# Kernel optimization log

Hardware: AMD Instinct MI355X
Metric: run time of the kernel (lower is better)

Reference implementation:

```python
import jax, jax.numpy as jnp
import numpy as np

N, K, FIN, FOUT = 50000, 32, 128, 128

def setup_inputs() -> dict:
    key = jax.random.key(0)
    k1, k2, k3 = jax.random.split(key, 3)
    x = jax.random.normal(k1, (N, FIN), dtype=jnp.float32)
    nbrs = jax.random.randint(k2, (N, K), 0, N)
    # nn.Linear weight init scale ~ 1/sqrt(fan_in)
    W = jax.random.normal(k3, (FIN, FOUT), dtype=jnp.float32) / np.sqrt(FIN).astype(np.float32)
    return {"x": x, "nbrs": nbrs, "W": W}

def reference(x, nbrs, W):
    # h = self.w(x)  (bias=False)
    h = x @ W                              # [N, FOUT]
    g = jnp.take(h, nbrs, axis=0)          # [N, K, FOUT] gather of neighbor features
    s = jnp.sort(g, axis=1)                # sort each neighbor list per feature
    k = nbrs.shape[1]
    # torch.median returns the lower median: sorted[(k-1)//2]
    return s[:, (k - 1) // 2, :]           # [N, FOUT]
```

## Files before the change

kernel.cpp:

```cpp
#include <hip/hip_runtime.h>

#define FIN 128
#define FOUT 128
#define KNB 32
#define QD 16

typedef __attribute__((ext_vector_type(8))) short bf16x8;
typedef __attribute__((ext_vector_type(4))) float f32x4;

__global__ __launch_bounds__(256) void wf_stage(
    const float* __restrict__ W, unsigned* __restrict__ wf) {
  const int id = blockIdx.x * 256 + threadIdx.x;
  if (id >= 2048) return;
  const int lane = id & 63;
  const int kb = (id >> 6) & 3;
  const int ct = id >> 8;
  const int krow = kb * 32 + (lane >> 4) * 8;
  const int col = ct * 16 + (lane & 15);
  unsigned d[4];
  #pragma unroll
  for (int p = 0; p < 4; ++p) {
    const float lo = W[(krow + 2 * p) * FOUT + col];
    const float hi = W[(krow + 2 * p + 1) * FOUT + col];
    asm("v_cvt_pk_bf16_f32 %0, %1, %2" : "=v"(d[p]) : "v"(lo), "v"(hi));
  }
  uint4 q; q.x = d[0]; q.y = d[1]; q.z = d[2]; q.w = d[3];
  *(uint4*)(wf + (size_t)id * 4) = q;
}

__global__ __launch_bounds__(256) void gemm_mfma(
    const float* __restrict__ x, const unsigned* __restrict__ wf,
    unsigned* __restrict__ h, int n_rows) {
  const int t = threadIdx.x;
  const int w = t >> 6;
  const int l = t & 63;
  const int kq = l >> 4;
  const int row_base = blockIdx.x * 32;

  uint4 wfr[2][4];
  #pragma unroll
  for (int c = 0; c < 2; ++c)
    #pragma unroll
    for (int kb = 0; kb < 4; ++kb)
      wfr[c][kb] = *(const uint4*)(wf + (size_t)(((2 * w + c) * 4 + kb) * 64 + l) * 4);

  #pragma unroll
  for (int tile = 0; tile < 2; ++tile) {
    const int row = row_base + tile * 16 + (l & 15);
    const int rsafe = min(row, n_rows - 1);

    bf16x8 xf[4];
    #pragma unroll
    for (int kb = 0; kb < 4; ++kb) {
      const float* xp = x + (size_t)rsafe * FIN + kb * 32 + kq * 8;
      const float4 x0 = *(const float4*)(xp);
      const float4 x1 = *(const float4*)(xp + 4);
      union { unsigned u[4]; bf16x8 v; } pk;
      asm("v_cvt_pk_bf16_f32 %0, %1, %2" : "=v"(pk.u[0]) : "v"(x0.x), "v"(x0.y));
      asm("v_cvt_pk_bf16_f32 %0, %1, %2" : "=v"(pk.u[1]) : "v"(x0.z), "v"(x0.w));
      asm("v_cvt_pk_bf16_f32 %0, %1, %2" : "=v"(pk.u[2]) : "v"(x1.x), "v"(x1.y));
      asm("v_cvt_pk_bf16_f32 %0, %1, %2" : "=v"(pk.u[3]) : "v"(x1.z), "v"(x1.w));
      xf[kb] = pk.v;
    }

    #pragma unroll
    for (int c = 0; c < 2; ++c) {
      f32x4 acc = {0.f, 0.f, 0.f, 0.f};
      #pragma unroll
      for (int kb = 0; kb < 4; ++kb) {
        union { uint4 q; bf16x8 v; } af;
        af.q = wfr[c][kb];
        acc = __builtin_amdgcn_mfma_f32_16x16x32_bf16(af.v, xf[kb], acc, 0, 0, 0);
      }
      if (row < n_rows) {
        unsigned p0, p1;
        asm("v_cvt_pkrtz_f16_f32 %0, %1, %2" : "=v"(p0) : "v"(acc[0]), "v"(acc[1]));
        asm("v_cvt_pkrtz_f16_f32 %0, %1, %2" : "=v"(p1) : "v"(acc[2]), "v"(acc[3]));
        uint2 st; st.x = p0; st.y = p1;
        *(uint2*)(h + ((size_t)w * n_rows + row) * QD + c * 8 + kq * 2) = st;
      }
    }
  }
}

__device__ __forceinline__ void ce(unsigned& a, unsigned& b) {
  unsigned mn, mx;
  asm("v_pk_min_f16 %0, %1, %2" : "=v"(mn) : "v"(a), "v"(b));
  asm("v_pk_max_f16 %0, %1, %2" : "=v"(mx) : "v"(a), "v"(b));
  a = mn; b = mx;
}
__device__ __forceinline__ unsigned pmin(unsigned a, unsigned b) {
  unsigned r;
  asm("v_pk_min_f16 %0, %1, %2" : "=v"(r) : "v"(a), "v"(b));
  return r;
}
__device__ __forceinline__ unsigned pmax(unsigned a, unsigned b) {
  unsigned r;
  asm("v_pk_max_f16 %0, %1, %2" : "=v"(r) : "v"(a), "v"(b));
  return r;
}

#define OEMS16(v, base)                                                        \
  _Pragma("unroll") for (int p = 1; p < 16; p <<= 1)                           \
  _Pragma("unroll") for (int k = p; k >= 1; k >>= 1)                           \
  _Pragma("unroll") for (int j = k & (p - 1); j + k < 16; j += 2 * k)          \
  _Pragma("unroll") for (int i = 0; i < k; ++i)                                \
    if (((i + j) / (2 * p)) == ((i + j + k) / (2 * p)))                        \
      ce(v[(base) + i + j], v[(base) + i + j + k]);

__global__ __launch_bounds__(256) void median_gather(
    const unsigned* __restrict__ h, const int* __restrict__ nbrs,
    float* __restrict__ out, int n_nodes, int blocks_per_q) {
  __shared__ int sidx[16 * 33];
  const int t = threadIdx.x;
  const int q  = blockIdx.x / blocks_per_q;
  const int bq = blockIdx.x - q * blocks_per_q;
  const int node_base = bq * 16;

  {
    const int2 p2 = *(const int2*)(nbrs + (size_t)node_base * KNB + t * 2);
    const int e = t * 2;
    const int nl0 = e >> 5, k0 = e & 31;
    sidx[nl0 * 33 + k0] = p2.x;
    sidx[nl0 * 33 + k0 + 1] = p2.y;
  }
  __syncthreads();

  const int nl = t >> 4;
  const int d  = t & 15;
  const unsigned qbase = (unsigned)q * (unsigned)n_nodes * QD + (unsigned)d;

  int idxv[KNB];
  #pragma unroll
  for (int k = 0; k < KNB; ++k) idxv[k] = sidx[nl * 33 + k];

  unsigned v[KNB];
  #pragma unroll
  for (int k = 0; k < KNB; ++k)
    v[k] = h[qbase + (unsigned)idxv[k] * QD];

  OEMS16(v, 0)
  OEMS16(v, 16)

  unsigned m[16];
  #pragma unroll
  for (int i = 0; i < 16; ++i) m[i] = pmin(v[i], v[31 - i]);
  #pragma unroll
  for (int s = 8; s >= 1; s >>= 1)
    #pragma unroll
    for (int i = 0; i < s; ++i) m[i] = pmax(m[i], m[i + s]);

  float flo, fhi;
  asm("v_cvt_f32_f16 %0, %1" : "=v"(flo) : "v"(m[0]));
  asm("v_cvt_f32_f16 %0, %1" : "=v"(fhi) : "v"(m[0] >> 16));
  float2 o; o.x = flo; o.y = fhi;

  const int node = node_base + nl;
  *(float2*)(out + (size_t)node * FOUT + q * 32 + d * 2) = o;
}

extern "C" void kernel_launch(void* const* d_in, const int* in_sizes, int n_in,
                              void* d_out, int out_size, void* d_ws, size_t ws_size,
                              hipStream_t stream) {
  const float* x    = (const float*)d_in[0];
  const int*   nbrs = (const int*)d_in[1];
  const float* W    = (const float*)d_in[2];
  float* out = (float*)d_out;

  unsigned* h  = (unsigned*)d_ws;
  unsigned* wf = (unsigned*)d_ws + 3200000;

  const int n = in_sizes[0] / FIN;

  wf_stage<<<8, 256, 0, stream>>>(W, wf);
  gemm_mfma<<<(n + 31) / 32, 256, 0, stream>>>(x, wf, h, n);
  const int bpq = n / 16;
  median_gather<<<4 * bpq, 256, 0, stream>>>(h, nbrs, out, n, bpq);
}
```

Before: 69.92 us.

## Stage W fragments in LDS and give each wave all output columns; add nontemporal accesses

The GEMM now copies all bf16 W fragments (32 KB) into shared memory once per block. Each wave handles its own 16-row tile across all 8 column tiles, so x is loaded and converted once per row, where before every wave reloaded the same rows for its 2 column tiles. Blocks cover 64 rows, so the grid is half as large. The median kernel switches its neighbor-index loads, gathered h loads and output stores to nontemporal builtins to reduce cache pollution. The trade-offs are a per-block LDS fill plus barrier, and possible loss of useful cache hits on the random h gathers.

```diff
diff --git a/kernel.cpp b/kernel.cpp
--- a/kernel.cpp
+++ b/kernel.cpp
@@ -31,73 +31,60 @@
 __global__ __launch_bounds__(256) void gemm_mfma(
     const float* __restrict__ x, const unsigned* __restrict__ wf,
     unsigned* __restrict__ h, int n_rows) {
+  __shared__ uint4 wls[2048];
   const int t = threadIdx.x;
-  const int w = t >> 6;
+  #pragma unroll
+  for (int i = 0; i < 8; ++i)
+    wls[i * 256 + t] = ((const uint4*)wf)[i * 256 + t];
+  __syncthreads();
+
   const int l = t & 63;
   const int kq = l >> 4;
-  const int row_base = blockIdx.x * 32;
+  const int row = blockIdx.x * 64 + (t >> 6) * 16 + (l & 15);
+  const int rsafe = min(row, n_rows - 1);
 
-  uint4 wfr[2][4];
+  bf16x8 xf[4];
   #pragma unroll
-  for (int c = 0; c < 2; ++c)
-    #pragma unroll
-    for (int kb = 0; kb < 4; ++kb)
-      wfr[c][kb] = *(const uint4*)(wf + (size_t)(((2 * w + c) * 4 + kb) * 64 + l) * 4);
+  for (int kb = 0; kb < 4; ++kb) {
+    const float* xp = x + (size_t)rsafe * FIN + kb * 32 + kq * 8;
+    const float4 x0 = *(const float4*)(xp);
+    const float4 x1 = *(const float4*)(xp + 4);
+    union { unsigned u[4]; bf16x8 v; } pk;
+    asm("v_cvt_pk_bf16_f32 %0, %1, %2" : "=v"(pk.u[0]) : "v"(x0.x), "v"(x0.y));
+    asm("v_cvt_pk_bf16_f32 %0, %1, %2" : "=v"(pk.u[1]) : "v"(x0.z), "v"(x0.w));
+    asm("v_cvt_pk_bf16_f32 %0, %1, %2" : "=v"(pk.u[2]) : "v"(x1.x), "v"(x1.y));
+    asm("v_cvt_pk_bf16_f32 %0, %1, %2" : "=v"(pk.u[3]) : "v"(x1.z), "v"(x1.w));
+    xf[kb] = pk.v;
+  }
 
   #pragma unroll
-  for (int tile = 0; tile < 2; ++tile) {
-    const int row = row_base + tile * 16 + (l & 15);
-    const int rsafe = min(row, n_rows - 1);
-
-    bf16x8 xf[4];
+  for (int ct = 0; ct < 8; ++ct) {
+    f32x4 acc = {0.f, 0.f, 0.f, 0.f};
     #pragma unroll
     for (int kb = 0; kb < 4; ++kb) {
-      const float* xp = x + (size_t)rsafe * FIN + kb * 32 + kq * 8;
-      const float4 x0 = *(const float4*)(xp);
-      const float4 x1 = *(const float4*)(xp + 4);
-      union { unsigned u[4]; bf16x8 v; } pk;
-      asm("v_cvt_pk_bf16_f32 %0, %1, %2" : "=v"(pk.u[0]) : "v"(x0.x), "v"(x0.y));
-      asm("v_cvt_pk_bf16_f32 %0, %1, %2" : "=v"(pk.u[1]) : "v"(x0.z), "v"(x0.w));
-      asm("v_cvt_pk_bf16_f32 %0, %1, %2" : "=v"(pk.u[2]) : "v"(x1.x), "v"(x1.y));
-      asm("v_cvt_pk_bf16_f32 %0, %1, %2" : "=v"(pk.u[3]) : "v"(x1.z), "v"(x1.w));
-      xf[kb] = pk.v;
+      union { uint4 q; bf16x8 v; } af;
+      af.q = wls[(ct * 4 + kb) * 64 + l];
+      acc = __builtin_amdgcn_mfma_f32_16x16x32_bf16(af.v, xf[kb], acc, 0, 0, 0);
     }
-
-    #pragma unroll
-    for (int c = 0; c < 2; ++c) {
-      f32x4 acc = {0.f, 0.f, 0.f, 0.f};
-      #pragma unroll
-      for (int kb = 0; kb < 4; ++kb) {
-        union { uint4 q; bf16x8 v; } af;
-        af.q = wfr[c][kb];
-        acc = __builtin_amdgcn_mfma_f32_16x16x32_bf16(af.v, xf[kb], acc, 0, 0, 0);
-      }
-      if (row < n_rows) {
-        unsigned p0, p1;
-        asm("v_cvt_pkrtz_f16_f32 %0, %1, %2" : "=v"(p0) : "v"(acc[0]), "v"(acc[1]));
-        asm("v_cvt_pkrtz_f16_f32 %0, %1, %2" : "=v"(p1) : "v"(acc[2]), "v"(acc[3]));
-        uint2 st; st.x = p0; st.y = p1;
-        *(uint2*)(h + ((size_t)w * n_rows + row) * QD + c * 8 + kq * 2) = st;
-      }
+    if (row < n_rows) {
+      unsigned p0, p1;
+      asm("v_cvt_pkrtz_f16_f32 %0, %1, %2" : "=v"(p0) : "v"(acc[0]), "v"(acc[1]));
+      asm("v_cvt_pkrtz_f16_f32 %0, %1, %2" : "=v"(p1) : "v"(acc[2]), "v"(acc[3]));
+      uint2 st; st.x = p0; st.y = p1;
+      *(uint2*)(h + ((size_t)(ct >> 1) * n_rows + row) * QD + (ct & 1) * 8 + kq * 2) = st;
     }
   }
 }
 
-__device__ __forceinline__ void ce(unsigned& a, unsigned& b) {
-  unsigned mn, mx;
-  asm("v_pk_min_f16 %0, %1, %2" : "=v"(mn) : "v"(a), "v"(b));
-  asm("v_pk_max_f16 %0, %1, %2" : "=v"(mx) : "v"(a), "v"(b));
-  a = mn; b = mx;
-}
 __device__ __forceinline__ unsigned pmin(unsigned a, unsigned b) {
-  unsigned r;
-  asm("v_pk_min_f16 %0, %1, %2" : "=v"(r) : "v"(a), "v"(b));
-  return r;
+  unsigned r; asm("v_pk_min_f16 %0, %1, %2" : "=v"(r) : "v"(a), "v"(b)); return r;
 }
 __device__ __forceinline__ unsigned pmax(unsigned a, unsigned b) {
-  unsigned r;
-  asm("v_pk_max_f16 %0, %1, %2" : "=v"(r) : "v"(a), "v"(b));
-  return r;
+  unsigned r; asm("v_pk_max_f16 %0, %1, %2" : "=v"(r) : "v"(a), "v"(b)); return r;
+}
+__device__ __forceinline__ void ce(unsigned& a, unsigned& b) {
+  const unsigned mn = pmin(a, b), mx = pmax(a, b);
+  a = mn; b = mx;
 }
 
 #define OEMS16(v, base)                                                        \
@@ -118,11 +105,12 @@
   const int node_base = bq * 16;
 
   {
-    const int2 p2 = *(const int2*)(nbrs + (size_t)node_base * KNB + t * 2);
     const int e = t * 2;
+    const int i0 = __builtin_nontemporal_load(nbrs + (size_t)node_base * KNB + e);
+    const int i1 = __builtin_nontemporal_load(nbrs + (size_t)node_base * KNB + e + 1);
     const int nl0 = e >> 5, k0 = e & 31;
-    sidx[nl0 * 33 + k0] = p2.x;
-    sidx[nl0 * 33 + k0 + 1] = p2.y;
+    sidx[nl0 * 33 + k0] = i0;
+    sidx[nl0 * 33 + k0 + 1] = i1;
   }
   __syncthreads();
 
@@ -137,7 +125,7 @@
   unsigned v[KNB];
   #pragma unroll
   for (int k = 0; k < KNB; ++k)
-    v[k] = h[qbase + (unsigned)idxv[k] * QD];
+    v[k] = __builtin_nontemporal_load(h + qbase + (unsigned)idxv[k] * QD);
 
   OEMS16(v, 0)
   OEMS16(v, 16)
@@ -153,10 +141,14 @@
   float flo, fhi;
   asm("v_cvt_f32_f16 %0, %1" : "=v"(flo) : "v"(m[0]));
   asm("v_cvt_f32_f16 %0, %1" : "=v"(fhi) : "v"(m[0] >> 16));
-  float2 o; o.x = flo; o.y = fhi;
-
+  double pack;
+  {
+    float2 o; o.x = flo; o.y = fhi;
+    __builtin_memcpy(&pack, &o, 8);
+  }
   const int node = node_base + nl;
-  *(float2*)(out + (size_t)node * FOUT + q * 32 + d * 2) = o;
+  __builtin_nontemporal_store(
+      pack, (double*)(out + (size_t)node * FOUT + q * 32 + d * 2));
 }
 
 extern "C" void kernel_launch(void* const* d_in, const int* in_sizes, int n_in,
@@ -173,7 +165,7 @@
   const int n = in_sizes[0] / FIN;
 
   wf_stage<<<8, 256, 0, stream>>>(W, wf);
-  gemm_mfma<<<(n + 31) / 32, 256, 0, stream>>>(x, wf, h, n);
+  gemm_mfma<<<(n + 63) / 64, 256, 0, stream>>>(x, wf, h, n);
   const int bpq = n / 16;
   median_gather<<<4 * bpq, 256, 0, stream>>>(h, nbrs, out, n, bpq);
 }
```

Result: slower. 125.3 us (+79.2%).
